# Kernel optimization log

Measured on AMD Instinct MI355X. Metric: run time of the kernel, lower is better.

The kernel has to match this reference:

```python
import jax, jax.numpy as jnp
import numpy as np
import math

HIDDEN = 1024
HEADS = 16
HEAD_DIM = HIDDEN // HEADS


def setup_inputs() -> dict:
    key = jax.random.key(0)
    ks = jax.random.split(key, 9)
    s = 1.0 / math.sqrt(HIDDEN)
    return {
        "x": jax.random.normal(ks[0], (4, 2048, HIDDEN), dtype=jnp.float32),
        "Wq": jax.random.normal(ks[1], (HIDDEN, HIDDEN), dtype=jnp.float32) * s,
        "bq": jnp.zeros((HIDDEN,), dtype=jnp.float32),
        "Wk": jax.random.normal(ks[2], (HIDDEN, HIDDEN), dtype=jnp.float32) * s,
        "bk": jnp.zeros((HIDDEN,), dtype=jnp.float32),
        "Wv": jax.random.normal(ks[3], (HIDDEN, HIDDEN), dtype=jnp.float32) * s,
        "bv": jnp.zeros((HIDDEN,), dtype=jnp.float32),
        "Wo": jax.random.normal(ks[4], (HIDDEN, HIDDEN), dtype=jnp.float32) * s,
        "bo": jnp.zeros((HIDDEN,), dtype=jnp.float32),
    }


def reference(x, Wq, bq, Wk, bk, Wv, bv, Wo, bo):
    B, L, D = x.shape
    H, hd = HEADS, HEAD_DIM
    # QKV projections (weights stored as [in, out], i.e. torch W.T)
    q = (x @ Wq + bq).reshape(B, L, H, hd).transpose(0, 2, 1, 3)  # [B,H,L,hd]
    k = (x @ Wk + bk).reshape(B, L, H, hd).transpose(0, 2, 1, 3)
    v = (x @ Wv + bv).reshape(B, L, H, hd).transpose(0, 2, 1, 3)
    scores = jnp.einsum("bhqd,bhkd->bhqk", q, k) / math.sqrt(hd)  # [B,H,L,L]
    causal_mask = jnp.triu(jnp.full((L, L), -jnp.inf, dtype=scores.dtype), k=1)
    att = jax.nn.softmax(scores + causal_mask, axis=-1)
    out = jnp.einsum("bhqk,bhkd->bhqd", att, v)  # [B,H,L,hd]
    out = out.transpose(0, 2, 1, 3).reshape(B, L, D)
    return out @ Wo + bo
```

## Files before the change

kernel.cpp:

```cpp
#include <hip/hip_runtime.h>
#include <stdint.h>

#define LOG2E 1.44269504088896340736f

typedef __attribute__((ext_vector_type(8))) short short8;
typedef __attribute__((ext_vector_type(4))) float float4v;

typedef const __attribute__((address_space(1))) unsigned int gu32;
typedef __attribute__((address_space(3))) unsigned int lu32;

__device__ __forceinline__ void async16(const unsigned short* g, unsigned short* l){
  __builtin_amdgcn_global_load_lds((gu32*)g, (lu32*)l, 16, 0, 0);
}

__device__ __forceinline__ unsigned short f2bf(float f){
  union { float f; unsigned int u; } v; v.f = f;
  unsigned int u = v.u;
  return (unsigned short)((u + 0x7FFFu + ((u >> 16) & 1u)) >> 16);
}
__device__ __forceinline__ unsigned int pkbf(float a, float b){
  union { float f; unsigned int u; } ua, ub; ua.f=a; ub.f=b;
  return ((ua.u + 0x8000u) >> 16) | ((ub.u + 0x8000u) & 0xFFFF0000u);
}

__global__ void convert_x_kernel(const float* __restrict__ x, unsigned short* __restrict__ xb){
  int t = blockIdx.x * 256 + threadIdx.x;
  const float4v* xp = (const float4v*)x;
  float4v a = xp[2*t], b = xp[2*t+1];
  short8 o;
  o[0]=(short)f2bf(a[0]); o[1]=(short)f2bf(a[1]); o[2]=(short)f2bf(a[2]); o[3]=(short)f2bf(a[3]);
  o[4]=(short)f2bf(b[0]); o[5]=(short)f2bf(b[1]); o[6]=(short)f2bf(b[2]); o[7]=(short)f2bf(b[3]);
  ((short8*)xb)[t] = o;
}

__global__ void transpose_w_kernel(const float* __restrict__ Wq, const float* __restrict__ Wk,
                                   const float* __restrict__ Wv, const float* __restrict__ Wo,
                                   unsigned short* __restrict__ wqkvT, unsigned short* __restrict__ woT){
  __shared__ float tileS[64][68];
  int mat = blockIdx.x >> 8, tile = blockIdx.x & 255;
  int tk = tile >> 4, tn = tile & 15;
  const float* W = (mat==0)?Wq:(mat==1)?Wk:(mat==2)?Wv:Wo;
  int k0 = tk*64, n0 = tn*64;
  int tid = threadIdx.x;
  #pragma unroll
  for (int it=0; it<4; ++it){
    int idx = tid + it*256;
    int r = idx >> 4, c4 = idx & 15;
    float4v v = *(const float4v*)&W[(uint64_t)(k0+r)*1024 + n0 + c4*4];
    tileS[r][c4*4+0]=v[0]; tileS[r][c4*4+1]=v[1]; tileS[r][c4*4+2]=v[2]; tileS[r][c4*4+3]=v[3];
  }
  __syncthreads();
  unsigned short* dst; int nbase;
  if (mat<3){ dst = wqkvT; nbase = mat*1024 + n0; } else { dst = woT; nbase = n0; }
  #pragma unroll
  for (int it=0; it<2; ++it){
    int idx = tid + it*256;
    int n = idx >> 3, g = idx & 7;
    short8 o;
    #pragma unroll
    for (int j=0;j<8;++j) o[j] = (short)f2bf(tileS[g*8+j][n]);
    *(short8*)&dst[(uint64_t)(nbase+n)*1024 + k0 + g*8] = o;
  }
}

__global__ void transpose_v_kernel(const unsigned short* __restrict__ v, unsigned short* __restrict__ vt){
  __shared__ __attribute__((aligned(16))) unsigned short t[64][72];
  int bh = blockIdx.x >> 5, lt = blockIdx.x & 31;
  int l0 = lt*64, tid = threadIdx.x;
  #pragma unroll
  for (int it=0; it<2; ++it){
    int idx = tid + it*256;
    int l = idx >> 3, g = idx & 7;
    short8 x = *(const short8*)&v[((uint64_t)bh*2048 + l0 + l)*64 + g*8];
    *(short8*)&t[l][g*8] = x;
  }
  __syncthreads();
  #pragma unroll
  for (int it=0; it<2; ++it){
    int idx = tid + it*256;
    int d = idx >> 3, g = idx & 7;
    short8 o;
    #pragma unroll
    for (int j=0;j<8;++j) o[j] = (short)t[g*8+j][d];
    *(short8*)&vt[((uint64_t)bh*64 + d)*2048 + l0 + g*8] = o;
  }
}

template<int EPI>
__global__ __launch_bounds__(256, 2) void gemm_kernel(
    const unsigned short* __restrict__ A, const unsigned short* __restrict__ BT,
    const float* __restrict__ bias0, const float* __restrict__ bias1, const float* __restrict__ bias2,
    unsigned short* __restrict__ oq, unsigned short* __restrict__ ok,
    unsigned short* __restrict__ ov, float* __restrict__ of)
{
  __shared__ __attribute__((aligned(16))) unsigned short lS[2*128*64];
  unsigned short* lA = lS;
  unsigned short* lB = lS + 128*64;
  const int tid = threadIdx.x, lane = tid & 63, wave = tid >> 6;
  const int wr = wave >> 1, wc = wave & 1;
  const int by = blockIdx.x & 63, bx = blockIdx.x >> 6;
  const int m0 = by * 128, n0 = bx * 128;
  const int c = lane & 15, quad = lane >> 4;
  const float QSCALE = 0.125f * LOG2E;

  float4v acc[4][4];
  #pragma unroll
  for (int i=0;i<4;++i)
    #pragma unroll
    for (int j=0;j<4;++j) acc[i][j] = (float4v){0.f,0.f,0.f,0.f};

  for (int kt = 0; kt < 16; ++kt){
    __syncthreads();
    #pragma unroll
    for (int it=0; it<4; ++it){
      int gl = (wave*4+it)*64 + lane;
      int row = gl >> 3, gp = gl & 7, gs = gp ^ (row & 7);
      async16(&A[(uint64_t)(m0+row)*1024 + kt*64 + gs*8], &lA[gl*8]);
    }
    #pragma unroll
    for (int it=0; it<4; ++it){
      int gl = (wave*4+it)*64 + lane;
      int row = gl >> 3, gp = gl & 7, gs = gp ^ (row & 7);
      async16(&BT[(uint64_t)(n0+row)*1024 + kt*64 + gs*8], &lB[gl*8]);
    }
    __syncthreads();
    #pragma unroll
    for (int kk=0; kk<2; ++kk){
      short8 af[4], bf[4];
      #pragma unroll
      for (int i=0;i<4;++i){
        int row = wr*64 + i*16 + c;
        int g = (quad + kk*4) ^ (row & 7);
        af[i] = *(const short8*)&lA[row*64 + g*8];
      }
      #pragma unroll
      for (int j=0;j<4;++j){
        int row = wc*64 + j*16 + c;
        int g = (quad + kk*4) ^ (row & 7);
        bf[j] = *(const short8*)&lB[row*64 + g*8];
      }
      #pragma unroll
      for (int i=0;i<4;++i)
        #pragma unroll
        for (int j=0;j<4;++j)
          acc[i][j] = __builtin_amdgcn_mfma_f32_16x16x32_bf16(af[i], bf[j], acc[i][j], 0, 0, 0);
    }
  }

  if (EPI == 0){
    const int sel = bx >> 3;
    const int n0l = n0 & 1023;
    const float* bp = (sel==0)?bias0:(sel==1)?bias1:bias2;
    unsigned short* dst = (sel==0)?oq:(sel==1)?ok:ov;
    float bj[4];
    #pragma unroll
    for (int j=0;j<4;++j) bj[j] = bp[n0l + wc*64 + j*16 + c];
    __syncthreads();
    #pragma unroll
    for (int i=0;i<4;++i){
      #pragma unroll
      for (int r=0;r<4;++r){
        int mloc = wr*64 + i*16 + quad*4 + r;
        #pragma unroll
        for (int j=0;j<4;++j){
          float v = acc[i][j][r] + bj[j];
          if (sel == 0) v *= QSCALE;
          int col = wc*64 + j*16 + c;
          int gg = col >> 3;
          int gs2 = (gg & 8) | ((gg & 7) ^ (mloc & 7));
          lS[mloc*128 + gs2*8 + (col & 7)] = f2bf(v);
        }
      }
    }
    __syncthreads();
    const int h0 = n0l >> 6;
    #pragma unroll
    for (int it=0; it<8; ++it){
      int gl = it*256 + tid;
      int row = gl >> 4, gg = gl & 15;
      int gs2 = (gg & 8) | ((gg & 7) ^ (row & 7));
      short8 w = *(const short8*)&lS[row*128 + gs2*8];
      int m = m0 + row;
      int bb = m >> 11, l = m & 2047;
      int hh = h0 + (gg >> 3);
      *(short8*)&dst[((uint64_t)(bb*16 + hh)*2048 + l)*64 + (gg & 7)*8] = w;
    }
  } else {
    float* lf = (float*)lS;
    float bj[4];
    #pragma unroll
    for (int j=0;j<4;++j) bj[j] = bias0[n0 + wc*64 + j*16 + c];
    #pragma unroll
    for (int half=0; half<2; ++half){
      __syncthreads();
      if (wr == half){
        #pragma unroll
        for (int i=0;i<4;++i){
          #pragma unroll
          for (int r=0;r<4;++r){
            int lrow = i*16 + quad*4 + r;
            #pragma unroll
            for (int j=0;j<4;++j){
              int col = wc*64 + j*16 + c;
              int gg = col >> 2;
              int gs2 = (gg & 24) | ((gg & 7) ^ (lrow & 7));
              lf[lrow*128 + gs2*4 + (col & 3)] = acc[i][j][r] + bj[j];
            }
          }
        }
      }
      __syncthreads();
      #pragma unroll
      for (int it=0; it<8; ++it){
        int gl = it*256 + tid;
        int lrow = gl >> 5, gg = gl & 31;
        int gs2 = (gg & 24) | ((gg & 7) ^ (lrow & 7));
        float4v w = *(const float4v*)&lf[lrow*128 + gs2*4];
        *(float4v*)&of[(uint64_t)(m0 + half*64 + lrow)*1024 + n0 + gg*4] = w;
      }
    }
  }
}

__global__ __launch_bounds__(256, 2) void attn_kernel(
    const unsigned short* __restrict__ q, const unsigned short* __restrict__ k,
    const unsigned short* __restrict__ vt, unsigned short* __restrict__ o)
{
  __shared__ __attribute__((aligned(16))) unsigned short lQ[128*64];
  __shared__ __attribute__((aligned(16))) unsigned short lK[2][64*64];
  __shared__ __attribute__((aligned(16))) unsigned short lV[2][64*64];
  __shared__ __attribute__((aligned(16))) unsigned short lP[4][32*64];

  const int idx = blockIdx.x;
  const int bh = idx & 63;
  const int qt = 15 - (idx >> 6);
  const int tid = threadIdx.x, lane = tid & 63, wave = tid >> 6;
  const int c = lane & 15, quad = lane >> 4;

  const unsigned short* qh = q  + (uint64_t)bh * (2048*64);
  const unsigned short* kh = k  + (uint64_t)bh * (2048*64);
  const unsigned short* vh = vt + (uint64_t)bh * (64*2048);

  #pragma unroll
  for (int it=0; it<4; ++it){
    int gl = (wave*4+it)*64 + lane;
    int row = gl >> 3, gp = gl & 7, gs = gp ^ (row & 7);
    async16(&qh[(uint64_t)(qt*128 + row)*64 + gs*8], &lQ[gl*8]);
  }
  #pragma unroll
  for (int it=0; it<2; ++it){
    int gl = (wave*2+it)*64 + lane;
    int row = gl >> 3, gp = gl & 7, gs = gp ^ (row & 7);
    async16(&kh[(uint64_t)row*64 + gs*8], &lK[0][gl*8]);
    async16(&vh[(uint64_t)row*2048 + gs*8], &lV[0][gl*8]);
  }

  float4v accO[2][4];
  #pragma unroll
  for (int u=0;u<2;++u)
    #pragma unroll
    for (int t=0;t<4;++t) accO[u][t] = (float4v){0.f,0.f,0.f,0.f};
  float lsum[2] = {0.f, 0.f};
  short8 qf[2][2];

  const int qbase = qt*128 + wave*32;
  const int ktEnd = 2*qt + 1;
  unsigned short* Pw = &lP[wave][0];

  for (int kt = 0; kt <= ktEnd; ++kt){
    __syncthreads();
    const int cb = kt & 1;

    if (kt == 0){
      #pragma unroll
      for (int u=0; u<2; ++u)
        #pragma unroll
        for (int kk=0; kk<2; ++kk){
          int row = wave*32 + u*16 + c;
          int g = (kk*4 + quad) ^ (row & 7);
          qf[u][kk] = *(const short8*)&lQ[row*64 + g*8];
        }
    }
    if (kt < ktEnd){
      const int nb = 1 - cb;
      #pragma unroll
      for (int it=0; it<2; ++it){
        int gl = (wave*2+it)*64 + lane;
        int row = gl >> 3, gp = gl & 7, gs = gp ^ (row & 7);
        async16(&kh[(uint64_t)((kt+1)*64 + row)*64 + gs*8], &lK[nb][gl*8]);
        async16(&vh[(uint64_t)row*2048 + (kt+1)*64 + gs*8], &lV[nb][gl*8]);
      }
    }

    if (kt*64 >= qbase + 32) continue;

    float4v s[2][4];
    #pragma unroll
    for (int u=0;u<2;++u)
      #pragma unroll
      for (int j=0;j<4;++j) s[u][j] = (float4v){0.f,0.f,0.f,0.f};
    #pragma unroll
    for (int kk=0; kk<2; ++kk){
      short8 kf[4];
      #pragma unroll
      for (int j=0;j<4;++j){
        int row = j*16 + c;
        int g = (kk*4 + quad) ^ (row & 7);
        kf[j] = *(const short8*)&lK[cb][row*64 + g*8];
      }
      #pragma unroll
      for (int u=0;u<2;++u)
        #pragma unroll
        for (int j=0;j<4;++j)
          s[u][j] = __builtin_amdgcn_mfma_f32_16x16x32_bf16(kf[j], qf[u][kk], s[u][j], 0, 0, 0);
    }

    const bool needMask = (kt*64 + 63 > qbase);
    #pragma unroll
    for (int u=0;u<2;++u){
      const int qg = qbase + u*16 + c;
      #pragma unroll
      for (int j=0;j<4;++j){
        float p0,p1,p2,p3;
        {
          float4v sv = s[u][j];
          p0 = __builtin_amdgcn_exp2f(sv[0]);
          p1 = __builtin_amdgcn_exp2f(sv[1]);
          p2 = __builtin_amdgcn_exp2f(sv[2]);
          p3 = __builtin_amdgcn_exp2f(sv[3]);
        }
        if (needMask){
          int keyb = kt*64 + j*16 + quad*4;
          if (keyb + 0 > qg) p0 = 0.f;
          if (keyb + 1 > qg) p1 = 0.f;
          if (keyb + 2 > qg) p2 = 0.f;
          if (keyb + 3 > qg) p3 = 0.f;
        }
        lsum[u] += (p0 + p1) + (p2 + p3);
        int row = u*16 + c;
        int g = (2*j + (quad>>1)) ^ (row & 7);
        uint2 w; w.x = pkbf(p0,p1); w.y = pkbf(p2,p3);
        *(uint2*)&Pw[row*64 + g*8 + (quad&1)*4] = w;
      }
    }

    #pragma unroll
    for (int kk=0; kk<2; ++kk){
      short8 bv[4];
      #pragma unroll
      for (int t=0;t<4;++t){
        int row = t*16 + c;
        int g = (kk*4 + quad) ^ (row & 7);
        bv[t] = *(const short8*)&lV[cb][row*64 + g*8];
      }
      #pragma unroll
      for (int u=0;u<2;++u){
        int row = u*16 + c;
        int g = (kk*4 + quad) ^ (row & 7);
        short8 ap = *(const short8*)&Pw[row*64 + g*8];
        #pragma unroll
        for (int t=0;t<4;++t)
          accO[u][t] = __builtin_amdgcn_mfma_f32_16x16x32_bf16(ap, bv[t], accO[u][t], 0, 0, 0);
      }
    }
  }

  #pragma unroll
  for (int u=0;u<2;++u){
    lsum[u] += __shfl_xor(lsum[u], 16, 64);
    lsum[u] += __shfl_xor(lsum[u], 32, 64);
  }

  const int b = bh >> 4, h = bh & 15;
  unsigned short* lPf = &lP[0][0];
  #pragma unroll
  for (int u=0;u<2;++u){
    #pragma unroll
    for (int r=0;r<4;++r){
      float ls = __shfl(lsum[u], quad*4 + r, 64);
      float rinv = 1.0f / ls;
      int mloc = wave*32 + u*16 + quad*4 + r;
      #pragma unroll
      for (int t=0;t<4;++t){
        int col = t*16 + c;
        int gg = col >> 3;
        int gs2 = gg ^ (mloc & 7);
        lPf[mloc*64 + gs2*8 + (col & 7)] = f2bf(accO[u][t][r] * rinv);
      }
    }
  }
  __syncthreads();
  #pragma unroll
  for (int it=0; it<4; ++it){
    int gl = it*256 + tid;
    int row = gl >> 3, gg = gl & 7;
    int gs2 = gg ^ (row & 7);
    short8 w = *(const short8*)&lPf[row*64 + gs2*8];
    uint64_t m = (uint64_t)b*2048 + qt*128 + row;
    *(short8*)&o[m*1024 + h*64 + gg*8] = w;
  }
}

extern "C" void kernel_launch(void* const* d_in, const int* in_sizes, int n_in,
                              void* d_out, int out_size, void* d_ws, size_t ws_size,
                              hipStream_t stream)
{
  (void)in_sizes; (void)n_in; (void)out_size; (void)ws_size;
  const float* x  = (const float*)d_in[0];
  const float* Wq = (const float*)d_in[1];
  const float* bq = (const float*)d_in[2];
  const float* Wk = (const float*)d_in[3];
  const float* bk = (const float*)d_in[4];
  const float* Wv = (const float*)d_in[5];
  const float* bv = (const float*)d_in[6];
  const float* Wo = (const float*)d_in[7];
  const float* bo = (const float*)d_in[8];
  float* out = (float*)d_out;

  char* ws = (char*)d_ws;
  unsigned short* xb    = (unsigned short*)(ws);
  unsigned short* wqkvT = (unsigned short*)(ws + (16ull<<20));
  unsigned short* woT   = (unsigned short*)(ws + (22ull<<20));
  unsigned short* qb    = (unsigned short*)(ws + (24ull<<20));
  unsigned short* kb    = (unsigned short*)(ws + (40ull<<20));
  unsigned short* vb    = (unsigned short*)(ws + (56ull<<20));
  unsigned short* vtb   = xb;
  unsigned short* ab    = vb;

  convert_x_kernel<<<4096, 256, 0, stream>>>(x, xb);
  transpose_w_kernel<<<1024, 256, 0, stream>>>(Wq, Wk, Wv, Wo, wqkvT, woT);
  gemm_kernel<0><<<1536, 256, 0, stream>>>(xb, wqkvT, bq, bk, bv, qb, kb, vb, nullptr);
  transpose_v_kernel<<<2048, 256, 0, stream>>>(vb, vtb);
  attn_kernel<<<1024, 256, 0, stream>>>(qb, kb, vtb, ab);
  gemm_kernel<1><<<512, 256, 0, stream>>>(ab, woT, bo, nullptr, nullptr, nullptr, nullptr, nullptr, out);
}
```

Before: 253.4 us.

## Fuse V transpose into QKV GEMM epilogue and interleave causal query rows

The QKV GEMM epilogue now writes V directly in transposed [bh, d, L] layout through a transposed LDS staging pattern, which removes the separate transpose_v kernel launch and its extra pass over V in memory. In the attention kernel, each wave's query rows are interleaved (u*64 + wave*16) instead of contiguous, so the causal workload is balanced across waves. The first row-group is skipped only on the final diagonal tile, replacing the per-wave early continue. Buffer aliasing is rearranged so the attention output reuses the x buffer.

```diff
diff --git a/kernel.cpp b/kernel.cpp
--- a/kernel.cpp
+++ b/kernel.cpp
@@ -60,29 +60,6 @@
     #pragma unroll
     for (int j=0;j<8;++j) o[j] = (short)f2bf(tileS[g*8+j][n]);
     *(short8*)&dst[(uint64_t)(nbase+n)*1024 + k0 + g*8] = o;
-  }
-}
-
-__global__ void transpose_v_kernel(const unsigned short* __restrict__ v, unsigned short* __restrict__ vt){
-  __shared__ __attribute__((aligned(16))) unsigned short t[64][72];
-  int bh = blockIdx.x >> 5, lt = blockIdx.x & 31;
-  int l0 = lt*64, tid = threadIdx.x;
-  #pragma unroll
-  for (int it=0; it<2; ++it){
-    int idx = tid + it*256;
-    int l = idx >> 3, g = idx & 7;
-    short8 x = *(const short8*)&v[((uint64_t)bh*2048 + l0 + l)*64 + g*8];
-    *(short8*)&t[l][g*8] = x;
-  }
-  __syncthreads();
-  #pragma unroll
-  for (int it=0; it<2; ++it){
-    int idx = tid + it*256;
-    int d = idx >> 3, g = idx & 7;
-    short8 o;
-    #pragma unroll
-    for (int j=0;j<8;++j) o[j] = (short)t[g*8+j][d];
-    *(short8*)&vt[((uint64_t)bh*64 + d)*2048 + l0 + g*8] = o;
   }
 }
 
@@ -150,40 +127,67 @@
   if (EPI == 0){
     const int sel = bx >> 3;
     const int n0l = n0 & 1023;
+    const int h0 = n0l >> 6;
+    const int bb = m0 >> 11, l0 = m0 & 2047;
     const float* bp = (sel==0)?bias0:(sel==1)?bias1:bias2;
-    unsigned short* dst = (sel==0)?oq:(sel==1)?ok:ov;
     float bj[4];
     #pragma unroll
     for (int j=0;j<4;++j) bj[j] = bp[n0l + wc*64 + j*16 + c];
     __syncthreads();
-    #pragma unroll
-    for (int i=0;i<4;++i){
-      #pragma unroll
-      for (int r=0;r<4;++r){
-        int mloc = wr*64 + i*16 + quad*4 + r;
-        #pragma unroll
-        for (int j=0;j<4;++j){
-          float v = acc[i][j][r] + bj[j];
-          if (sel == 0) v *= QSCALE;
-          int col = wc*64 + j*16 + c;
-          int gg = col >> 3;
-          int gs2 = (gg & 8) | ((gg & 7) ^ (mloc & 7));
-          lS[mloc*128 + gs2*8 + (col & 7)] = f2bf(v);
-        }
-      }
-    }
-    __syncthreads();
-    const int h0 = n0l >> 6;
-    #pragma unroll
-    for (int it=0; it<8; ++it){
-      int gl = it*256 + tid;
-      int row = gl >> 4, gg = gl & 15;
-      int gs2 = (gg & 8) | ((gg & 7) ^ (row & 7));
-      short8 w = *(const short8*)&lS[row*128 + gs2*8];
-      int m = m0 + row;
-      int bb = m >> 11, l = m & 2047;
-      int hh = h0 + (gg >> 3);
-      *(short8*)&dst[((uint64_t)(bb*16 + hh)*2048 + l)*64 + (gg & 7)*8] = w;
+    if (sel < 2){
+      unsigned short* dst = (sel==0)?oq:ok;
+      #pragma unroll
+      for (int i=0;i<4;++i){
+        #pragma unroll
+        for (int r=0;r<4;++r){
+          int mloc = wr*64 + i*16 + quad*4 + r;
+          #pragma unroll
+          for (int j=0;j<4;++j){
+            float v = acc[i][j][r] + bj[j];
+            if (sel == 0) v *= QSCALE;
+            int col = wc*64 + j*16 + c;
+            int gg = col >> 3;
+            int gs2 = (gg & 8) | ((gg & 7) ^ (mloc & 7));
+            lS[mloc*128 + gs2*8 + (col & 7)] = f2bf(v);
+          }
+        }
+      }
+      __syncthreads();
+      #pragma unroll
+      for (int it=0; it<8; ++it){
+        int gl = it*256 + tid;
+        int row = gl >> 4, gg = gl & 15;
+        int gs2 = (gg & 8) | ((gg & 7) ^ (row & 7));
+        short8 w = *(const short8*)&lS[row*128 + gs2*8];
+        int hh = h0 + (gg >> 3);
+        *(short8*)&dst[((uint64_t)(bb*16 + hh)*2048 + l0 + row)*64 + (gg & 7)*8] = w;
+      }
+    } else {
+      #pragma unroll
+      for (int i=0;i<4;++i){
+        #pragma unroll
+        for (int r=0;r<4;++r){
+          int mloc = wr*64 + i*16 + quad*4 + r;
+          int mgg = mloc >> 3;
+          #pragma unroll
+          for (int j=0;j<4;++j){
+            float v = acc[i][j][r] + bj[j];
+            int col = wc*64 + j*16 + c;
+            int gsT = (mgg & 8) | ((mgg & 7) ^ (col & 7));
+            lS[col*128 + gsT*8 + (mloc & 7)] = f2bf(v);
+          }
+        }
+      }
+      __syncthreads();
+      #pragma unroll
+      for (int it=0; it<8; ++it){
+        int idx = it*256 + tid;
+        int mg = idx & 15, cc = idx >> 4;
+        int gsT2 = (mg & 8) | ((mg & 7) ^ (cc & 7));
+        short8 w = *(const short8*)&lS[cc*128 + gsT2*8];
+        int hh = h0 + (cc >> 6), d = cc & 63;
+        *(short8*)&ov[((uint64_t)(bb*16 + hh)*64 + d)*2048 + l0 + mg*8] = w;
+      }
     }
   } else {
     float* lf = (float*)lS;
@@ -263,7 +267,6 @@
   float lsum[2] = {0.f, 0.f};
   short8 qf[2][2];
 
-  const int qbase = qt*128 + wave*32;
   const int ktEnd = 2*qt + 1;
   unsigned short* Pw = &lP[wave][0];
 
@@ -276,7 +279,7 @@
       for (int u=0; u<2; ++u)
         #pragma unroll
         for (int kk=0; kk<2; ++kk){
-          int row = wave*32 + u*16 + c;
+          int row = u*64 + wave*16 + c;
           int g = (kk*4 + quad) ^ (row & 7);
           qf[u][kk] = *(const short8*)&lQ[row*64 + g*8];
         }
@@ -292,7 +295,7 @@
       }
     }
 
-    if (kt*64 >= qbase + 32) continue;
+    const bool doU0 = (kt != ktEnd);
 
     float4v s[2][4];
     #pragma unroll
@@ -309,16 +312,21 @@
         kf[j] = *(const short8*)&lK[cb][row*64 + g*8];
       }
       #pragma unroll
-      for (int u=0;u<2;++u)
+      for (int j=0;j<4;++j)
+        s[1][j] = __builtin_amdgcn_mfma_f32_16x16x32_bf16(kf[j], qf[1][kk], s[1][j], 0, 0, 0);
+      if (doU0){
         #pragma unroll
         for (int j=0;j<4;++j)
-          s[u][j] = __builtin_amdgcn_mfma_f32_16x16x32_bf16(kf[j], qf[u][kk], s[u][j], 0, 0, 0);
-    }
-
-    const bool needMask = (kt*64 + 63 > qbase);
+          s[0][j] = __builtin_amdgcn_mfma_f32_16x16x32_bf16(kf[j], qf[0][kk], s[0][j], 0, 0, 0);
+      }
+    }
+
     #pragma unroll
     for (int u=0;u<2;++u){
-      const int qg = qbase + u*16 + c;
+      if (u==0 && !doU0) continue;
+      const int qb_u = qt*128 + u*64 + wave*16;
+      const bool needMask = (kt*64 + 63 > qb_u);
+      const int qg = qb_u + c;
       #pragma unroll
       for (int j=0;j<4;++j){
         float p0,p1,p2,p3;
@@ -353,14 +361,21 @@
         int g = (kk*4 + quad) ^ (row & 7);
         bv[t] = *(const short8*)&lV[cb][row*64 + g*8];
       }
-      #pragma unroll
-      for (int u=0;u<2;++u){
-        int row = u*16 + c;
+      {
+        int row = 16 + c;
         int g = (kk*4 + quad) ^ (row & 7);
         short8 ap = *(const short8*)&Pw[row*64 + g*8];
         #pragma unroll
         for (int t=0;t<4;++t)
-          accO[u][t] = __builtin_amdgcn_mfma_f32_16x16x32_bf16(ap, bv[t], accO[u][t], 0, 0, 0);
+          accO[1][t] = __builtin_amdgcn_mfma_f32_16x16x32_bf16(ap, bv[t], accO[1][t], 0, 0, 0);
+      }
+      if (doU0){
+        int row = c;
+        int g = (kk*4 + quad) ^ (row & 7);
+        short8 ap = *(const short8*)&Pw[row*64 + g*8];
+        #pragma unroll
+        for (int t=0;t<4;++t)
+          accO[0][t] = __builtin_amdgcn_mfma_f32_16x16x32_bf16(ap, bv[t], accO[0][t], 0, 0, 0);
       }
     }
   }
@@ -379,7 +394,7 @@
     for (int r=0;r<4;++r){
       float ls = __shfl(lsum[u], quad*4 + r, 64);
       float rinv = 1.0f / ls;
-      int mloc = wave*32 + u*16 + quad*4 + r;
+      int mloc = u*64 + wave*16 + quad*4 + r;
       #pragma unroll
       for (int t=0;t<4;++t){
         int col = t*16 + c;
@@ -423,14 +438,12 @@
   unsigned short* woT   = (unsigned short*)(ws + (22ull<<20));
   unsigned short* qb    = (unsigned short*)(ws + (24ull<<20));
   unsigned short* kb    = (unsigned short*)(ws + (40ull<<20));
-  unsigned short* vb    = (unsigned short*)(ws + (56ull<<20));
-  unsigned short* vtb   = xb;
-  unsigned short* ab    = vb;
+  unsigned short* vtb   = (unsigned short*)(ws + (56ull<<20));
+  unsigned short* ab    = xb;
 
   convert_x_kernel<<<4096, 256, 0, stream>>>(x, xb);
   transpose_w_kernel<<<1024, 256, 0, stream>>>(Wq, Wk, Wv, Wo, wqkvT, woT);
-  gemm_kernel<0><<<1536, 256, 0, stream>>>(xb, wqkvT, bq, bk, bv, qb, kb, vb, nullptr);
-  transpose_v_kernel<<<2048, 256, 0, stream>>>(vb, vtb);
+  gemm_kernel<0><<<1536, 256, 0, stream>>>(xb, wqkvT, bq, bk, bv, qb, kb, vtb, nullptr);
   attn_kernel<<<1024, 256, 0, stream>>>(qb, kb, vtb, ab);
   gemm_kernel<1><<<512, 256, 0, stream>>>(ab, woT, bo, nullptr, nullptr, nullptr, nullptr, nullptr, out);
 }
```

After: 247.4 us. 1.02x faster.
